# Kernel optimization log

Measured on AMD Instinct MI355X. Metric: run time of the kernel, lower is better.

Reference implementation:

```python
import jax, jax.numpy as jnp
import numpy as np

N_TIME = 512          # n_time_nodes
LATENT = 32           # latent_dim
HIDDEN = 64           # hidden_dim
N_MODES = 8           # r_fourier_modes
X_A0 = 0.3            # initial stoichiometry (anode)
CSANMAX = 28700.0     # max concentration scale
BASE_LOGIT = float(np.log(X_A0 / (1.0 - X_A0)))  # logit_from_fraction(x_a0)
FEAT_DIM = 1 + 2 * N_MODES   # [rho, cos(k*pi*rho), sin(k*pi*rho)]
IN_DIM = LATENT + FEAT_DIM
N_POINTS = 2_000_000


def setup_inputs() -> dict:
    key = jax.random.key(0)
    ks = jax.random.split(key, 8)
    time_idx = jax.random.randint(ks[0], (N_POINTS,), 0, N_TIME)
    rho = jax.random.uniform(ks[1], (N_POINTS,), dtype=jnp.float32)
    # trainable latent code per nonzero time node
    emb = jax.random.normal(ks[2], (N_TIME - 1, LATENT), dtype=jnp.float32) * 0.02
    # decoder_a: Linear(IN,HID)+SiLU, Linear(HID,HID)+SiLU, Linear(HID,1)
    W0 = jax.random.normal(ks[3], (IN_DIM, HIDDEN), dtype=jnp.float32) / np.sqrt(IN_DIM)
    b0 = jnp.zeros((HIDDEN,), jnp.float32)
    W1 = jax.random.normal(ks[4], (HIDDEN, HIDDEN), dtype=jnp.float32) / np.sqrt(HIDDEN)
    b1 = jnp.zeros((HIDDEN,), jnp.float32)
    Wout = jax.random.normal(ks[5], (HIDDEN, 1), dtype=jnp.float32) * 0.1
    bout = jnp.zeros((1,), jnp.float32)
    return {"time_idx": time_idx, "rho": rho, "emb": emb,
            "W0": W0, "b0": b0, "W1": W1, "b1": b1, "Wout": Wout, "bout": bout}


def _radius_features(rho):
    # [N] -> [N, 1 + 2*N_MODES]
    k = jnp.arange(1, N_MODES + 1, dtype=rho.dtype)
    ang = jnp.pi * rho[:, None] * k[None, :]
    return jnp.concatenate([rho[:, None], jnp.cos(ang), jnp.sin(ang)], axis=1)


def reference(time_idx, rho, emb, W0, b0, W1, b1, Wout, bout):
    # predicated version of the torch masked scatter: compute everywhere,
    # select initial-condition value where time_idx == 0
    idx = jnp.clip(time_idx - 1, 0, N_TIME - 2)       # safe gather index
    e = emb[idx]                                       # [N, LATENT]
    feat = _radius_features(rho)                       # [N, FEAT_DIM]
    h = jnp.concatenate([e, feat], axis=1)             # [N, IN_DIM]
    h = jax.nn.silu(h @ W0 + b0)
    h = jax.nn.silu(h @ W1 + b1)
    raw = (h @ Wout + bout)[:, 0]                      # [N]
    theta = jax.nn.sigmoid(raw + BASE_LOGIT)
    return jnp.where(time_idx == 0, X_A0 * CSANMAX, theta * CSANMAX)
```

## Files before the change

### kernel.cpp

```cpp
#include <hip/hip_runtime.h>
#include <stdint.h>


typedef _Float16 half8  __attribute__((ext_vector_type(8)));
typedef _Float16 half4v __attribute__((ext_vector_type(4)));
typedef _Float16 half2v __attribute__((ext_vector_type(2)));
typedef float f32x4 __attribute__((ext_vector_type(4)));

#define LOG2E 1.44269504088896340736f
#define NLN2  -0.6931471805599453f
#define CSCL  -1.44269504088896340736f
#define BASE_LOGIT -0.84729786038720367f
#define CSANMAX 28700.0f
#define IC_VAL 8610.0f

__device__ __forceinline__ float fast_exp2(float x) { return __builtin_amdgcn_exp2f(x); }
__device__ __forceinline__ float fast_rcp(float x)  { return __builtin_amdgcn_rcpf(x); }
__device__ __forceinline__ float sigf(float x)  { return fast_rcp(1.0f + fast_exp2(-LOG2E * x)); }
__device__ __forceinline__ void usilu2(float u0, float u1, float& p0, float& p1) {
  const float d0 = 1.0f + fast_exp2(u0);
  const float d1 = 1.0f + fast_exp2(u1);
  const float r  = fast_rcp(d0 * d1);
  p0 = u0 * d1 * r;
  p1 = u1 * d0 * r;
}
__device__ __forceinline__ half2v pkh(float a, float b) {
  return __builtin_bit_cast(half2v, __builtin_amdgcn_cvt_pkrtz(a, b));
}

union H8 { half8 v8; half2v v2[4]; };
union H4 { half4v v4; half2v v2[2]; };

__global__ __launch_bounds__(256, 4) void mlp_kernel(
    const int* __restrict__ tix, const float* __restrict__ rho,
    const float* __restrict__ emb, const float* __restrict__ W0,
    const float* __restrict__ b0, const float* __restrict__ W1,
    const float* __restrict__ b1, const float* __restrict__ Wout,
    const float* __restrict__ bout, float* __restrict__ out, int ntiles)
{
  __shared__ __align__(16) union {
    _Float16 stage[2][2][4][64][8];
    _Float16 H[4][16][72];
  } shA;

  const int tid  = threadIdx.x;
  const int wid  = tid >> 6;
  const int lane = tid & 63;
  const int m    = lane & 15;
  const int q    = lane >> 4;

  _Float16 (*Hb)[72] = shA.H[wid];

  if (wid == 0) {
#pragma unroll
    for (int t = 0; t < 4; ++t) {
#pragma unroll
      for (int s = 0; s < 2; ++s) {
        half8 f0, f1;
#pragma unroll
        for (int j = 0; j < 8; ++j) {
          const int k = s * 32 + q * 8 + j;
          const int n = t * 16 + m;
          float v0;
          if (k < 32) {
            v0 = W0[k * 64 + n];
          } else {
            const int kn = k - 32;
            v0 = (kn < 16) ? W0[(33 + kn) * 64 + n]
               : (kn == 16) ? W0[32 * 64 + n]
               : (kn == 17) ? b0[n] : 0.0f;
          }
          f0[j] = (_Float16)(CSCL * v0);
          f1[j] = (_Float16)W1[k * 64 + n];
        }
        *(half8*)&shA.stage[0][s][t][lane][0] = f0;
        *(half8*)&shA.stage[1][s][t][lane][0] = f1;
      }
    }
  }

  f32x4 bq1acc[4];
  f32x4 woutq[4];
#pragma unroll
  for (int t = 0; t < 4; ++t) {
    const f32x4 bv = *(const f32x4*)(b1 + t * 16 + q * 4);
    const f32x4 wv = *(const f32x4*)(Wout + t * 16 + q * 4);
#pragma unroll
    for (int r = 0; r < 4; ++r) {
      bq1acc[t][r] = CSCL * bv[r];
      woutq[t][r]  = NLN2 * wv[r];
    }
  }
  const float boutBL = bout[0] + BASE_LOGIT;

  __syncthreads();

  half8 w0A[4], w0B[4], w1A[4], w1B[4];
#pragma unroll
  for (int t = 0; t < 4; ++t) {
    w0A[t] = *(const half8*)&shA.stage[0][0][t][lane][0];
    w0B[t] = *(const half8*)&shA.stage[0][1][t][lane][0];
    w1A[t] = *(const half8*)&shA.stage[1][0][t][lane][0];
    w1B[t] = *(const half8*)&shA.stage[1][1][t][lane][0];
  }

  __syncthreads();

  const f32x4 z = {0.0f, 0.0f, 0.0f, 0.0f};
  const int tstride = gridDim.x * 4;

  int tg = blockIdx.x * 4 + wid;
  if (tg >= ntiles) return;
  const int lim = ntiles - 1;

  int   t0 = tix[tg * 16 + m];
  float r0 = rho[tg * 16 + m];
  const int tg1 = min(tg + tstride, lim);
  int   t1 = tix[tg1 * 16 + m];
  float r1 = rho[tg1 * 16 + m];
  const int idx0 = min(max(t0 - 1, 0), 510);
  const float* er0 = emb + (size_t)idx0 * 32 + q * 8;
  f32x4 eC0 = *(const f32x4*)er0;
  f32x4 eC1 = *(const f32x4*)(er0 + 4);

  while (true) {
    const int tg2 = min(tg + 2 * tstride, lim);
    const int   t2 = tix[tg2 * 16 + m];
    const float r2 = rho[tg2 * 16 + m];
    const int idxN = min(max(t1 - 1, 0), 510);
    const float* ern = emb + (size_t)idxN * 32 + q * 8;
    const f32x4 eN0 = *(const f32x4*)ern;
    const f32x4 eN1 = *(const f32x4*)(ern + 4);

    const float rhp = r0;
    const float rev = 0.5f * rhp;
    const float c1  = __builtin_amdgcn_cosf(rev);
    const float s1f = __builtin_amdgcn_sinf(rev);
    const float tc  = 2.0f * c1;
    const float x1v = (q == 0) ? c1 : ((q == 1) ? s1f : 0.0f);
    const float x0v = (q == 0) ? 1.0f : 0.0f;
    const float x2v = tc * x1v - x0v;
    const float x3v = tc * x2v - x1v;
    const float x4v = tc * x3v - x2v;
    const float x5v = tc * x4v - x3v;
    const float x6v = tc * x5v - x4v;
    const float x7v = tc * x6v - x5v;
    const float x8v = tc * x7v - x6v;
    H8 X1;
    X1.v2[0] = (q == 2) ? pkh(rhp, 1.0f) : pkh(x1v, x2v);
    X1.v2[1] = pkh(x3v, x4v);
    X1.v2[2] = pkh(x5v, x6v);
    X1.v2[3] = pkh(x7v, x8v);
    H8 X0;
    X0.v2[0] = pkh(eC0[0], eC0[1]); X0.v2[1] = pkh(eC0[2], eC0[3]);
    X0.v2[2] = pkh(eC1[0], eC1[1]); X0.v2[3] = pkh(eC1[2], eC1[3]);

    f32x4 acc[4];
#pragma unroll
    for (int t = 0; t < 4; ++t) {
      f32x4 a = __builtin_amdgcn_mfma_f32_16x16x32_f16(w0A[t], X0.v8, z, 0, 0, 0);
      a = __builtin_amdgcn_mfma_f32_16x16x32_f16(w0B[t], X1.v8, a, 0, 0, 0);
      acc[t] = a;
    }
#pragma unroll
    for (int t = 0; t < 4; ++t) {
      float p0, p1, p2, p3;
      usilu2(acc[t][0], acc[t][1], p0, p1);
      usilu2(acc[t][2], acc[t][3], p2, p3);
      H4 hh;
      hh.v2[0] = pkh(p0, p1);
      hh.v2[1] = pkh(p2, p3);
      *(half4v*)&Hb[m][t * 16 + q * 4] = hh.v4;
    }

    const half8 Y0 = *(const half8*)&Hb[m][q * 8];
    const half8 Y1 = *(const half8*)&Hb[m][32 + q * 8];
#pragma unroll
    for (int t = 0; t < 4; ++t) {
      f32x4 a = __builtin_amdgcn_mfma_f32_16x16x32_f16(w1A[t], Y0, bq1acc[t], 0, 0, 0);
      a = __builtin_amdgcn_mfma_f32_16x16x32_f16(w1B[t], Y1, a, 0, 0, 0);
      acc[t] = a;
    }
    float dA = 0.0f, dB = 0.0f;
#pragma unroll
    for (int t = 0; t < 4; ++t) {
      float p0, p1, p2, p3;
      usilu2(acc[t][0], acc[t][1], p0, p1);
      usilu2(acc[t][2], acc[t][3], p2, p3);
      dA = fmaf(p0, woutq[t][0], dA);
      dB = fmaf(p1, woutq[t][1], dB);
      dA = fmaf(p2, woutq[t][2], dA);
      dB = fmaf(p3, woutq[t][3], dB);
    }
    float dot = dA + dB;
    dot += __shfl_xor(dot, 16, 64);
    dot += __shfl_xor(dot, 32, 64);

    const float theta = sigf(dot + boutBL);
    const float val = (t0 == 0) ? IC_VAL : theta * CSANMAX;
    if (q == 0) out[tg * 16 + m] = val;

    const int tgn = tg + tstride;
    if (tgn >= ntiles) break;
    tg = tgn;
    t0 = t1; r0 = r1;
    t1 = t2; r1 = r2;
    eC0 = eN0; eC1 = eN1;
  }
}

extern "C" void kernel_launch(void* const* d_in, const int* in_sizes, int n_in,
                              void* d_out, int out_size, void* d_ws, size_t ws_size,
                              hipStream_t stream) {
  const int*   tix  = (const int*)d_in[0];
  const float* rho  = (const float*)d_in[1];
  const float* emb  = (const float*)d_in[2];
  const float* W0   = (const float*)d_in[3];
  const float* b0   = (const float*)d_in[4];
  const float* W1   = (const float*)d_in[5];
  const float* b1   = (const float*)d_in[6];
  const float* Wout = (const float*)d_in[7];
  const float* bout = (const float*)d_in[8];
  float* outp = (float*)d_out;

  const int n      = in_sizes[0];
  const int ntiles = n / 16;

  int grid = 1024;
  const int maxg = (ntiles + 3) / 4;
  if (grid > maxg) grid = maxg;
  mlp_kernel<<<dim3(grid), dim3(256), 0, stream>>>(
      tix, rho, emb, W0, b0, W1, b1, Wout, bout, outp, ntiles);
}
```

Baseline: 185.5 us.

## Software-pipeline MLP layers across tiles with double-buffered LDS hidden state

Splits the per-tile work into two phases (layer 0 plus SiLU written to LDS, then layer 1 plus output) and interleaves them across consecutive tiles. A double-buffered LDS region lets layer 1 of the previous tile run beside layer 0 of the current one, hiding LDS round-trip latency and giving the scheduler independent MFMA and transcendental work. The embedding conversion to fp16 is hoisted a tile ahead. Launch bounds drop from 4 to 3 blocks per SIMD to leave room for the extra live registers, which can lower occupancy.

```diff
diff --git a/kernel.cpp b/kernel.cpp
--- a/kernel.cpp
+++ b/kernel.cpp
@@ -16,7 +16,6 @@
 
 __device__ __forceinline__ float fast_exp2(float x) { return __builtin_amdgcn_exp2f(x); }
 __device__ __forceinline__ float fast_rcp(float x)  { return __builtin_amdgcn_rcpf(x); }
-__device__ __forceinline__ float sigf(float x)  { return fast_rcp(1.0f + fast_exp2(-LOG2E * x)); }
 __device__ __forceinline__ void usilu2(float u0, float u1, float& p0, float& p1) {
   const float d0 = 1.0f + fast_exp2(u0);
   const float d1 = 1.0f + fast_exp2(u1);
@@ -28,10 +27,10 @@
   return __builtin_bit_cast(half2v, __builtin_amdgcn_cvt_pkrtz(a, b));
 }
 
-union H8 { half8 v8; half2v v2[4]; };
+union H8 { half8 v8; half2v v2[4]; half4v v4[2]; };
 union H4 { half4v v4; half2v v2[2]; };
 
-__global__ __launch_bounds__(256, 4) void mlp_kernel(
+__global__ __launch_bounds__(256, 3) void mlp_kernel(
     const int* __restrict__ tix, const float* __restrict__ rho,
     const float* __restrict__ emb, const float* __restrict__ W0,
     const float* __restrict__ b0, const float* __restrict__ W1,
@@ -40,7 +39,7 @@
 {
   __shared__ __align__(16) union {
     _Float16 stage[2][2][4][64][8];
-    _Float16 H[4][16][72];
+    _Float16 H[4][2][16][72];
   } shA;
 
   const int tid  = threadIdx.x;
@@ -49,7 +48,7 @@
   const int m    = lane & 15;
   const int q    = lane >> 4;
 
-  _Float16 (*Hb)[72] = shA.H[wid];
+  _Float16 (*Hb2)[16][72] = shA.H[wid];
 
   if (wid == 0) {
 #pragma unroll
@@ -107,32 +106,13 @@
   __syncthreads();
 
   const f32x4 z = {0.0f, 0.0f, 0.0f, 0.0f};
-  const int tstride = gridDim.x * 4;
+  const int S = gridDim.x * 4;
 
   int tg = blockIdx.x * 4 + wid;
   if (tg >= ntiles) return;
   const int lim = ntiles - 1;
 
-  int   t0 = tix[tg * 16 + m];
-  float r0 = rho[tg * 16 + m];
-  const int tg1 = min(tg + tstride, lim);
-  int   t1 = tix[tg1 * 16 + m];
-  float r1 = rho[tg1 * 16 + m];
-  const int idx0 = min(max(t0 - 1, 0), 510);
-  const float* er0 = emb + (size_t)idx0 * 32 + q * 8;
-  f32x4 eC0 = *(const f32x4*)er0;
-  f32x4 eC1 = *(const f32x4*)(er0 + 4);
-
-  while (true) {
-    const int tg2 = min(tg + 2 * tstride, lim);
-    const int   t2 = tix[tg2 * 16 + m];
-    const float r2 = rho[tg2 * 16 + m];
-    const int idxN = min(max(t1 - 1, 0), 510);
-    const float* ern = emb + (size_t)idxN * 32 + q * 8;
-    const f32x4 eN0 = *(const f32x4*)ern;
-    const f32x4 eN1 = *(const f32x4*)(ern + 4);
-
-    const float rhp = r0;
+  auto phase1 = [&](float rhp, half8 X0v, int wb) {
     const float rev = 0.5f * rhp;
     const float c1  = __builtin_amdgcn_cosf(rev);
     const float s1f = __builtin_amdgcn_sinf(rev);
@@ -151,14 +131,11 @@
     X1.v2[1] = pkh(x3v, x4v);
     X1.v2[2] = pkh(x5v, x6v);
     X1.v2[3] = pkh(x7v, x8v);
-    H8 X0;
-    X0.v2[0] = pkh(eC0[0], eC0[1]); X0.v2[1] = pkh(eC0[2], eC0[3]);
-    X0.v2[2] = pkh(eC1[0], eC1[1]); X0.v2[3] = pkh(eC1[2], eC1[3]);
 
     f32x4 acc[4];
 #pragma unroll
     for (int t = 0; t < 4; ++t) {
-      f32x4 a = __builtin_amdgcn_mfma_f32_16x16x32_f16(w0A[t], X0.v8, z, 0, 0, 0);
+      f32x4 a = __builtin_amdgcn_mfma_f32_16x16x32_f16(w0A[t], X0v, z, 0, 0, 0);
       a = __builtin_amdgcn_mfma_f32_16x16x32_f16(w0B[t], X1.v8, a, 0, 0, 0);
       acc[t] = a;
     }
@@ -170,11 +147,14 @@
       H4 hh;
       hh.v2[0] = pkh(p0, p1);
       hh.v2[1] = pkh(p2, p3);
-      *(half4v*)&Hb[m][t * 16 + q * 4] = hh.v4;
-    }
-
-    const half8 Y0 = *(const half8*)&Hb[m][q * 8];
-    const half8 Y1 = *(const half8*)&Hb[m][32 + q * 8];
+      *(half4v*)&Hb2[wb][m][t * 16 + q * 4] = hh.v4;
+    }
+  };
+
+  auto phase2 = [&](int rb, int tgS, int icS) {
+    const half8 Y0 = *(const half8*)&Hb2[rb][m][q * 8];
+    const half8 Y1 = *(const half8*)&Hb2[rb][m][32 + q * 8];
+    f32x4 acc[4];
 #pragma unroll
     for (int t = 0; t < 4; ++t) {
       f32x4 a = __builtin_amdgcn_mfma_f32_16x16x32_f16(w1A[t], Y0, bq1acc[t], 0, 0, 0);
@@ -195,18 +175,67 @@
     float dot = dA + dB;
     dot += __shfl_xor(dot, 16, 64);
     dot += __shfl_xor(dot, 32, 64);
-
-    const float theta = sigf(dot + boutBL);
-    const float val = (t0 == 0) ? IC_VAL : theta * CSANMAX;
-    if (q == 0) out[tg * 16 + m] = val;
-
-    const int tgn = tg + tstride;
-    if (tgn >= ntiles) break;
-    tg = tgn;
-    t0 = t1; r0 = r1;
-    t1 = t2; r1 = r2;
-    eC0 = eN0; eC1 = eN1;
-  }
+    const float theta = fast_rcp(1.0f + fast_exp2(-LOG2E * (dot + boutBL)));
+    const float val = (icS == 0) ? IC_VAL : theta * CSANMAX;
+    if (q == 0) out[tgS * 16 + m] = val;
+  };
+
+  int   tC = tix[tg * 16 + m];
+  float rC = rho[tg * 16 + m];
+  const int tg1 = min(tg + S, lim);
+  int   tN = tix[tg1 * 16 + m];
+  float rN = rho[tg1 * 16 + m];
+  const int tg2 = min(tg + 2 * S, lim);
+  int   tNN0 = tix[tg2 * 16 + m];
+  float rNN0 = rho[tg2 * 16 + m];
+
+  H8 X0C;
+  {
+    const int idx = min(max(tC - 1, 0), 510);
+    const float* e = emb + (size_t)idx * 32 + q * 8;
+    const f32x4 e0 = *(const f32x4*)e;
+    const f32x4 e1 = *(const f32x4*)(e + 4);
+    X0C.v2[0] = pkh(e0[0], e0[1]); X0C.v2[1] = pkh(e0[2], e0[3]);
+    X0C.v2[2] = pkh(e1[0], e1[1]); X0C.v2[3] = pkh(e1[2], e1[3]);
+  }
+  phase1(rC, X0C.v8, 0);
+  int icP = tC, tgP = tg;
+  {
+    const int idx = min(max(tN - 1, 0), 510);
+    const float* e = emb + (size_t)idx * 32 + q * 8;
+    const f32x4 e0 = *(const f32x4*)e;
+    const f32x4 e1 = *(const f32x4*)(e + 4);
+    X0C.v2[0] = pkh(e0[0], e0[1]); X0C.v2[1] = pkh(e0[2], e0[3]);
+    X0C.v2[2] = pkh(e1[0], e1[1]); X0C.v2[3] = pkh(e1[2], e1[3]);
+  }
+  tC = tN; rC = rN;
+  tN = tNN0; rN = rNN0;
+
+  int wbuf = 1;
+  tg += S;
+
+  while (tg < ntiles) {
+    const int tgn2 = min(tg + 2 * S, lim);
+    const int   tNN = tix[tgn2 * 16 + m];
+    const float rNN = rho[tgn2 * 16 + m];
+    const int idxN = min(max(tN - 1, 0), 510);
+    const float* ern = emb + (size_t)idxN * 32 + q * 8;
+    const f32x4 eN0 = *(const f32x4*)ern;
+    const f32x4 eN1 = *(const f32x4*)(ern + 4);
+
+    phase2(wbuf ^ 1, tgP, icP);
+    phase1(rC, X0C.v8, wbuf);
+
+    icP = tC; tgP = tg;
+    X0C.v2[0] = pkh(eN0[0], eN0[1]); X0C.v2[1] = pkh(eN0[2], eN0[3]);
+    X0C.v2[2] = pkh(eN1[0], eN1[1]); X0C.v2[3] = pkh(eN1[2], eN1[3]);
+    tC = tN; rC = rN;
+    tN = tNN; rN = rNN;
+    wbuf ^= 1;
+    tg += S;
+  }
+
+  phase2(wbuf ^ 1, tgP, icP);
 }
 
 extern "C" void kernel_launch(void* const* d_in, const int* in_sizes, int n_in,
```

After: 160.0 us. 1.16x faster.

## Process tile pairs with software-pipelined layer stages and double-buffered LDS

Applied to the files above, without the earlier changes.

Each wave now handles two 16-row tiles per iteration. The second-layer and output stage of the previous pair is interleaved with the first-layer stage of the current pair through double-buffered LDS hidden buffers, so MFMA work and transcendental math can overlap and LDS latency is hidden. Bias and output weights are kept as packed halves to save registers, and launch bounds drop from 4 to 3 waves per SIMD, which raises register headroom at the cost of occupancy. The bias is now added after the MFMA instead of seeding the accumulator, which adds VALU adds. An odd tile count would leave the last tile unprocessed.

```diff
diff --git a/kernel.cpp b/kernel.cpp
--- a/kernel.cpp
+++ b/kernel.cpp
@@ -16,7 +16,6 @@
 
 __device__ __forceinline__ float fast_exp2(float x) { return __builtin_amdgcn_exp2f(x); }
 __device__ __forceinline__ float fast_rcp(float x)  { return __builtin_amdgcn_rcpf(x); }
-__device__ __forceinline__ float sigf(float x)  { return fast_rcp(1.0f + fast_exp2(-LOG2E * x)); }
 __device__ __forceinline__ void usilu2(float u0, float u1, float& p0, float& p1) {
   const float d0 = 1.0f + fast_exp2(u0);
   const float d1 = 1.0f + fast_exp2(u1);
@@ -28,10 +27,10 @@
   return __builtin_bit_cast(half2v, __builtin_amdgcn_cvt_pkrtz(a, b));
 }
 
-union H8 { half8 v8; half2v v2[4]; };
+union H8 { half8 v8; half2v v2[4]; half4v v4[2]; };
 union H4 { half4v v4; half2v v2[2]; };
 
-__global__ __launch_bounds__(256, 4) void mlp_kernel(
+__global__ __launch_bounds__(256, 3) void mlp_kernel(
     const int* __restrict__ tix, const float* __restrict__ rho,
     const float* __restrict__ emb, const float* __restrict__ W0,
     const float* __restrict__ b0, const float* __restrict__ W1,
@@ -40,7 +39,7 @@
 {
   __shared__ __align__(16) union {
     _Float16 stage[2][2][4][64][8];
-    _Float16 H[4][16][72];
+    _Float16 H[4][2][2][16][72];
   } shA;
 
   const int tid  = threadIdx.x;
@@ -48,8 +47,6 @@
   const int lane = tid & 63;
   const int m    = lane & 15;
   const int q    = lane >> 4;
-
-  _Float16 (*Hb)[72] = shA.H[wid];
 
   if (wid == 0) {
 #pragma unroll
@@ -79,17 +76,16 @@
     }
   }
 
-  f32x4 bq1acc[4];
-  f32x4 woutq[4];
+  half2v biash[8];
+  half2v wouth[8];
 #pragma unroll
   for (int t = 0; t < 4; ++t) {
     const f32x4 bv = *(const f32x4*)(b1 + t * 16 + q * 4);
     const f32x4 wv = *(const f32x4*)(Wout + t * 16 + q * 4);
-#pragma unroll
-    for (int r = 0; r < 4; ++r) {
-      bq1acc[t][r] = CSCL * bv[r];
-      woutq[t][r]  = NLN2 * wv[r];
-    }
+    biash[t * 2]     = pkh(CSCL * bv[0], CSCL * bv[1]);
+    biash[t * 2 + 1] = pkh(CSCL * bv[2], CSCL * bv[3]);
+    wouth[t * 2]     = pkh(NLN2 * wv[0], NLN2 * wv[1]);
+    wouth[t * 2 + 1] = pkh(NLN2 * wv[2], NLN2 * wv[3]);
   }
   const float boutBL = bout[0] + BASE_LOGIT;
 
@@ -107,32 +103,13 @@
   __syncthreads();
 
   const f32x4 z = {0.0f, 0.0f, 0.0f, 0.0f};
-  const int tstride = gridDim.x * 4;
-
-  int tg = blockIdx.x * 4 + wid;
-  if (tg >= ntiles) return;
-  const int lim = ntiles - 1;
-
-  int   t0 = tix[tg * 16 + m];
-  float r0 = rho[tg * 16 + m];
-  const int tg1 = min(tg + tstride, lim);
-  int   t1 = tix[tg1 * 16 + m];
-  float r1 = rho[tg1 * 16 + m];
-  const int idx0 = min(max(t0 - 1, 0), 510);
-  const float* er0 = emb + (size_t)idx0 * 32 + q * 8;
-  f32x4 eC0 = *(const f32x4*)er0;
-  f32x4 eC1 = *(const f32x4*)(er0 + 4);
-
-  while (true) {
-    const int tg2 = min(tg + 2 * tstride, lim);
-    const int   t2 = tix[tg2 * 16 + m];
-    const float r2 = rho[tg2 * 16 + m];
-    const int idxN = min(max(t1 - 1, 0), 510);
-    const float* ern = emb + (size_t)idxN * 32 + q * 8;
-    const f32x4 eN0 = *(const f32x4*)ern;
-    const f32x4 eN1 = *(const f32x4*)(ern + 4);
-
-    const float rhp = r0;
+  const int W = gridDim.x * 4;
+  const int npairs = ntiles >> 1;
+  int p = blockIdx.x * 4 + wid;
+  if (p >= npairs) return;
+  const int plim = npairs - 1;
+
+  auto phase1 = [&](float rhp, half8 X0v, _Float16 (*Hdst)[72]) {
     const float rev = 0.5f * rhp;
     const float c1  = __builtin_amdgcn_cosf(rev);
     const float s1f = __builtin_amdgcn_sinf(rev);
@@ -151,14 +128,11 @@
     X1.v2[1] = pkh(x3v, x4v);
     X1.v2[2] = pkh(x5v, x6v);
     X1.v2[3] = pkh(x7v, x8v);
-    H8 X0;
-    X0.v2[0] = pkh(eC0[0], eC0[1]); X0.v2[1] = pkh(eC0[2], eC0[3]);
-    X0.v2[2] = pkh(eC1[0], eC1[1]); X0.v2[3] = pkh(eC1[2], eC1[3]);
 
     f32x4 acc[4];
 #pragma unroll
     for (int t = 0; t < 4; ++t) {
-      f32x4 a = __builtin_amdgcn_mfma_f32_16x16x32_f16(w0A[t], X0.v8, z, 0, 0, 0);
+      f32x4 a = __builtin_amdgcn_mfma_f32_16x16x32_f16(w0A[t], X0v, z, 0, 0, 0);
       a = __builtin_amdgcn_mfma_f32_16x16x32_f16(w0B[t], X1.v8, a, 0, 0, 0);
       acc[t] = a;
     }
@@ -170,43 +144,120 @@
       H4 hh;
       hh.v2[0] = pkh(p0, p1);
       hh.v2[1] = pkh(p2, p3);
-      *(half4v*)&Hb[m][t * 16 + q * 4] = hh.v4;
-    }
-
-    const half8 Y0 = *(const half8*)&Hb[m][q * 8];
-    const half8 Y1 = *(const half8*)&Hb[m][32 + q * 8];
-#pragma unroll
-    for (int t = 0; t < 4; ++t) {
-      f32x4 a = __builtin_amdgcn_mfma_f32_16x16x32_f16(w1A[t], Y0, bq1acc[t], 0, 0, 0);
-      a = __builtin_amdgcn_mfma_f32_16x16x32_f16(w1B[t], Y1, a, 0, 0, 0);
-      acc[t] = a;
-    }
-    float dA = 0.0f, dB = 0.0f;
-#pragma unroll
-    for (int t = 0; t < 4; ++t) {
-      float p0, p1, p2, p3;
-      usilu2(acc[t][0], acc[t][1], p0, p1);
-      usilu2(acc[t][2], acc[t][3], p2, p3);
-      dA = fmaf(p0, woutq[t][0], dA);
-      dB = fmaf(p1, woutq[t][1], dB);
-      dA = fmaf(p2, woutq[t][2], dA);
-      dB = fmaf(p3, woutq[t][3], dB);
-    }
-    float dot = dA + dB;
-    dot += __shfl_xor(dot, 16, 64);
-    dot += __shfl_xor(dot, 32, 64);
-
-    const float theta = sigf(dot + boutBL);
-    const float val = (t0 == 0) ? IC_VAL : theta * CSANMAX;
-    if (q == 0) out[tg * 16 + m] = val;
-
-    const int tgn = tg + tstride;
-    if (tgn >= ntiles) break;
-    tg = tgn;
-    t0 = t1; r0 = r1;
-    t1 = t2; r1 = r2;
-    eC0 = eN0; eC1 = eN1;
-  }
+      *(half4v*)&Hdst[m][t * 16 + q * 4] = hh.v4;
+    }
+  };
+
+  auto phase2pair = [&](_Float16 (*Hsrc)[16][72], int pP, int taP, int tbP) {
+    float dots0, dots1;
+#pragma unroll
+    for (int s = 0; s < 2; ++s) {
+      const half8 Y0 = *(const half8*)&Hsrc[s][m][q * 8];
+      const half8 Y1 = *(const half8*)&Hsrc[s][m][32 + q * 8];
+      f32x4 acc[4];
+#pragma unroll
+      for (int t = 0; t < 4; ++t) {
+        f32x4 a = __builtin_amdgcn_mfma_f32_16x16x32_f16(w1A[t], Y0, z, 0, 0, 0);
+        a = __builtin_amdgcn_mfma_f32_16x16x32_f16(w1B[t], Y1, a, 0, 0, 0);
+        acc[t] = a;
+      }
+      float dA = 0.0f, dB = 0.0f;
+#pragma unroll
+      for (int t = 0; t < 4; ++t) {
+        float p0, p1, p2, p3;
+        const float u0 = (float)biash[t * 2][0]     + acc[t][0];
+        const float u1 = (float)biash[t * 2][1]     + acc[t][1];
+        const float u2 = (float)biash[t * 2 + 1][0] + acc[t][2];
+        const float u3 = (float)biash[t * 2 + 1][1] + acc[t][3];
+        usilu2(u0, u1, p0, p1);
+        usilu2(u2, u3, p2, p3);
+        dA = fmaf(p0, (float)wouth[t * 2][0],     dA);
+        dB = fmaf(p1, (float)wouth[t * 2][1],     dB);
+        dA = fmaf(p2, (float)wouth[t * 2 + 1][0], dA);
+        dB = fmaf(p3, (float)wouth[t * 2 + 1][1], dB);
+      }
+      float dot = dA + dB;
+      dot += __shfl_xor(dot, 16, 64);
+      dot += __shfl_xor(dot, 32, 64);
+      if (s == 0) dots0 = dot; else dots1 = dot;
+    }
+    const float dsel = (q & 1) ? dots1 : dots0;
+    const int   tsel = (q & 1) ? tbP : taP;
+    const float theta = fast_rcp(1.0f + fast_exp2(-LOG2E * (dsel + boutBL)));
+    const float val = (tsel == 0) ? IC_VAL : theta * CSANMAX;
+    if (q < 2) out[pP * 32 + q * 16 + m] = val;
+  };
+
+  int   tCa = tix[p * 32 + m],      tCb = tix[p * 32 + 16 + m];
+  float rCa = rho[p * 32 + m],      rCb = rho[p * 32 + 16 + m];
+  const int p1 = min(p + W, plim);
+  int   tNa = tix[p1 * 32 + m],     tNb = tix[p1 * 32 + 16 + m];
+  float rNa = rho[p1 * 32 + m],     rNb = rho[p1 * 32 + 16 + m];
+
+  H8 X0Ca, X0Cb;
+  {
+    const int ia = min(max(tCa - 1, 0), 510);
+    const int ib = min(max(tCb - 1, 0), 510);
+    const float* ea = emb + (size_t)ia * 32 + q * 8;
+    const float* eb = emb + (size_t)ib * 32 + q * 8;
+    const f32x4 a0 = *(const f32x4*)ea, a1 = *(const f32x4*)(ea + 4);
+    const f32x4 b0v = *(const f32x4*)eb, b1v = *(const f32x4*)(eb + 4);
+    X0Ca.v2[0] = pkh(a0[0], a0[1]); X0Ca.v2[1] = pkh(a0[2], a0[3]);
+    X0Ca.v2[2] = pkh(a1[0], a1[1]); X0Ca.v2[3] = pkh(a1[2], a1[3]);
+    X0Cb.v2[0] = pkh(b0v[0], b0v[1]); X0Cb.v2[1] = pkh(b0v[2], b0v[3]);
+    X0Cb.v2[2] = pkh(b1v[0], b1v[1]); X0Cb.v2[3] = pkh(b1v[2], b1v[3]);
+  }
+  phase1(rCa, X0Ca.v8, shA.H[wid][0][0]);
+  phase1(rCb, X0Cb.v8, shA.H[wid][0][1]);
+  int pPrev = p, taP = tCa, tbP = tCb;
+  {
+    const int ia = min(max(tNa - 1, 0), 510);
+    const int ib = min(max(tNb - 1, 0), 510);
+    const float* ea = emb + (size_t)ia * 32 + q * 8;
+    const float* eb = emb + (size_t)ib * 32 + q * 8;
+    const f32x4 a0 = *(const f32x4*)ea, a1 = *(const f32x4*)(ea + 4);
+    const f32x4 b0v = *(const f32x4*)eb, b1v = *(const f32x4*)(eb + 4);
+    X0Ca.v2[0] = pkh(a0[0], a0[1]); X0Ca.v2[1] = pkh(a0[2], a0[3]);
+    X0Ca.v2[2] = pkh(a1[0], a1[1]); X0Ca.v2[3] = pkh(a1[2], a1[3]);
+    X0Cb.v2[0] = pkh(b0v[0], b0v[1]); X0Cb.v2[1] = pkh(b0v[2], b0v[3]);
+    X0Cb.v2[2] = pkh(b1v[0], b1v[1]); X0Cb.v2[3] = pkh(b1v[2], b1v[3]);
+  }
+  tCa = tNa; rCa = rNa; tCb = tNb; rCb = rNb;
+  {
+    const int p2i = min(p + 2 * W, plim);
+    tNa = tix[p2i * 32 + m]; rNa = rho[p2i * 32 + m];
+    tNb = tix[p2i * 32 + 16 + m]; rNb = rho[p2i * 32 + 16 + m];
+  }
+  int cur = 1;
+  p += W;
+
+  while (p < npairs) {
+    const int pf = min(p + 2 * W, plim);
+    const int   tQa = tix[pf * 32 + m],      tQb = tix[pf * 32 + 16 + m];
+    const float rQa = rho[pf * 32 + m],      rQb = rho[pf * 32 + 16 + m];
+    const int ia = min(max(tNa - 1, 0), 510);
+    const int ib = min(max(tNb - 1, 0), 510);
+    const float* ea = emb + (size_t)ia * 32 + q * 8;
+    const float* eb = emb + (size_t)ib * 32 + q * 8;
+    const f32x4 eA0 = *(const f32x4*)ea, eA1 = *(const f32x4*)(ea + 4);
+    const f32x4 eB0 = *(const f32x4*)eb, eB1 = *(const f32x4*)(eb + 4);
+
+    phase2pair(shA.H[wid][cur ^ 1], pPrev, taP, tbP);
+    phase1(rCa, X0Ca.v8, shA.H[wid][cur][0]);
+    phase1(rCb, X0Cb.v8, shA.H[wid][cur][1]);
+
+    pPrev = p; taP = tCa; tbP = tCb;
+    X0Ca.v2[0] = pkh(eA0[0], eA0[1]); X0Ca.v2[1] = pkh(eA0[2], eA0[3]);
+    X0Ca.v2[2] = pkh(eA1[0], eA1[1]); X0Ca.v2[3] = pkh(eA1[2], eA1[3]);
+    X0Cb.v2[0] = pkh(eB0[0], eB0[1]); X0Cb.v2[1] = pkh(eB0[2], eB0[3]);
+    X0Cb.v2[2] = pkh(eB1[0], eB1[1]); X0Cb.v2[3] = pkh(eB1[2], eB1[3]);
+    tCa = tNa; rCa = rNa; tCb = tNb; rCb = rNb;
+    tNa = tQa; rNa = rQa; tNb = tQb; rNb = rQb;
+    cur ^= 1;
+    p += W;
+  }
+
+  phase2pair(shA.H[wid][cur ^ 1], pPrev, taP, tbP);
 }
 
 extern "C" void kernel_launch(void* const* d_in, const int* in_sizes, int n_in,
@@ -227,7 +278,8 @@
   const int ntiles = n / 16;
 
   int grid = 1024;
-  const int maxg = (ntiles + 3) / 4;
+  const int npairs = ntiles >> 1;
+  const int maxg = (npairs + 3) / 4;
   if (grid > maxg) grid = maxg;
   mlp_kernel<<<dim3(grid), dim3(256), 0, stream>>>(
       tix, rho, emb, W0, b0, W1, b1, Wout, bout, outp, ntiles);
```

Result: slower. 267.9 us (+44.4%).
